# Kernel tuning notes

Measured on AMD Instinct MI355X. Metric: run time of the kernel, lower is better.

The kernel has to match this reference:

```python
import jax, jax.numpy as jnp
import numpy as np
import math

B, N, F_IN, F_OUT = 16, 2048, 256, 64


def setup_inputs() -> dict:
    key = jax.random.key(0)
    k1, k2, k3, k4 = jax.random.split(key, 4)
    x = jax.random.normal(k1, (B, N, F_IN), dtype=jnp.float32)
    adj = jax.random.randint(k2, (B, N, N), 0, 2, dtype=jnp.int32)
    stdv = 1.0 / math.sqrt(F_OUT)
    weight = jax.random.uniform(k3, (F_IN, F_OUT), dtype=jnp.float32, minval=-stdv, maxval=stdv)
    # weight2 stdv = 1/sqrt(1) = 1.0
    weight2 = jax.random.uniform(k4, (2 * F_OUT, 1), dtype=jnp.float32, minval=-1.0, maxval=1.0)
    return {"x": x, "adj": adj, "weight": weight, "weight2": weight2}


def reference(x, adj, weight, weight2):
    # h[b,n,o] = (x @ weight)  -- shared linear projection
    h = jnp.einsum("bni,io->bno", x, weight)
    Fo = weight.shape[1]
    # Split additive-attention vector: e_ij = relu(h_i . a_src + h_j . a_dst)
    # Mathematically identical to cat([h_i, h_j]) @ weight2 of the original.
    a_src = weight2[:Fo, 0]
    a_dst = weight2[Fo:, 0]
    s_src = jnp.einsum("bno,o->bn", h, a_src)  # [B, N]
    s_dst = jnp.einsum("bno,o->bn", h, a_dst)  # [B, N]
    e = jax.nn.relu(s_src[:, :, None] + s_dst[:, None, :])  # [B, N, N]
    NEG = jnp.float32(-9e15)
    scores = jnp.where(adj > 0, e, NEG)
    attention = jax.nn.softmax(scores, axis=2)  # softmax over neighbors j
    # dropout = 0.0 / eval mode -> identity
    out = jnp.einsum("bij,bjo->bio", attention, h)  # [B, N, F_OUT]
    return out
```

## Files before the change

### kernel.cpp

```cpp
#include <hip/hip_runtime.h>
#include <hip/hip_bf16.h>

#define BB 16
#define NN 2048
#define FIN 256
#define FO 64
#define CH 256
#define HSTR 264

typedef __bf16 bf16x8 __attribute__((ext_vector_type(8)));
typedef float  f32x4  __attribute__((ext_vector_type(4)));
typedef int    i32x4  __attribute__((ext_vector_type(4)));
typedef unsigned int uint;

__global__ __launch_bounds__(256) void k1_gemm(
    const float* __restrict__ x, const float* __restrict__ weight,
    const float* __restrict__ w2,
    __bf16* __restrict__ hT, float* __restrict__ s_src, float* __restrict__ s_dst) {
    __shared__ __bf16 WtL[FO * 264];
    __shared__ float vsL[FIN], vdL[FIN];
    int t = threadIdx.x;
    {
        const float4* wr = (const float4*)(weight + t * FO);
        float a = 0.f, d = 0.f;
#pragma unroll
        for (int c = 0; c < 16; ++c) {
            float4 v = wr[c];
            int o = c * 4;
            WtL[(o + 0) * 264 + t] = (__bf16)v.x;
            WtL[(o + 1) * 264 + t] = (__bf16)v.y;
            WtL[(o + 2) * 264 + t] = (__bf16)v.z;
            WtL[(o + 3) * 264 + t] = (__bf16)v.w;
            a += v.x * w2[o] + v.y * w2[o + 1] + v.z * w2[o + 2] + v.w * w2[o + 3];
            d += v.x * w2[FO + o] + v.y * w2[FO + o + 1] +
                 v.z * w2[FO + o + 2] + v.w * w2[FO + o + 3];
        }
        vsL[t] = a;
        vdL[t] = d;
    }
    __syncthreads();

    int lane = threadIdx.x & 63, w = threadIdx.x >> 6;
    int quad = lane >> 4, m = lane & 15;
    int Rbase = blockIdx.x * 64 + w * 16;
    int R = Rbase + m;
    const float* xr = x + (long)R * FIN;

    f32x4 acc[4] = {};
    float ps = 0.f, pd = 0.f;

#pragma unroll
    for (int k0 = 0; k0 < FIN; k0 += 32) {
        int kb = k0 + quad * 8;
        float4 x0 = *(const float4*)(xr + kb);
        float4 x1 = *(const float4*)(xr + kb + 4);
        float4 u0 = *(const float4*)(vsL + kb);
        float4 u1 = *(const float4*)(vsL + kb + 4);
        float4 t0 = *(const float4*)(vdL + kb);
        float4 t1 = *(const float4*)(vdL + kb + 4);
        ps += x0.x * u0.x + x0.y * u0.y + x0.z * u0.z + x0.w * u0.w +
              x1.x * u1.x + x1.y * u1.y + x1.z * u1.z + x1.w * u1.w;
        pd += x0.x * t0.x + x0.y * t0.y + x0.z * t0.z + x0.w * t0.w +
              x1.x * t1.x + x1.y * t1.y + x1.z * t1.z + x1.w * t1.w;
        bf16x8 bf = {(__bf16)x0.x, (__bf16)x0.y, (__bf16)x0.z, (__bf16)x0.w,
                     (__bf16)x1.x, (__bf16)x1.y, (__bf16)x1.z, (__bf16)x1.w};
#pragma unroll
        for (int ot = 0; ot < 4; ++ot) {
            bf16x8 af = *(const bf16x8*)(WtL + (ot * 16 + m) * 264 + kb);
            acc[ot] = __builtin_amdgcn_mfma_f32_16x16x32_bf16(af, bf, acc[ot], 0, 0, 0);
        }
    }
    ps += __shfl_xor(ps, 16);
    ps += __shfl_xor(ps, 32);
    pd += __shfl_xor(pd, 16);
    pd += __shfl_xor(pd, 32);
    if (quad == 0) {
        s_src[R] = ps;
        s_dst[R] = pd;
    }
    int b = R >> 11;
    int nb = Rbase & (NN - 1);
#pragma unroll
    for (int ot = 0; ot < 4; ++ot) {
#pragma unroll
        for (int r = 0; r < 4; ++r) {
            int o = ot * 16 + quad * 4 + r;
            hT[((long)b * FO + o) * NN + nb + m] = (__bf16)acc[ot][r];
        }
    }
}

__global__ __launch_bounds__(256, 2) void k2_attn(
    const int* __restrict__ adj, const float* __restrict__ s_src,
    const float* __restrict__ s_dst, const __bf16* __restrict__ hT,
    float* __restrict__ out) {
    __shared__ __bf16 hL[2][FO * HSTR];
    __shared__ float EL[NN];
    int b = blockIdx.x >> 5;
    int i0 = (blockIdx.x & 31) << 6;
    int lane = threadIdx.x & 63, w = threadIdx.x >> 6;
    int quad = lane >> 4, m = lane & 15;
    int rowbase = i0 + w * 16;
    int row = rowbase + m;

    const float* sd = s_dst + b * NN;
    float mx = -3.0e38f;
    for (int j = lane; j < NN; j += 64) mx = fmaxf(mx, sd[j]);
#pragma unroll
    for (int off = 32; off >= 1; off >>= 1) mx = fmaxf(mx, __shfl_xor(mx, off));
    {
        int j0 = threadIdx.x * 8;
        float4 v0 = *(const float4*)(sd + j0);
        float4 v1 = *(const float4*)(sd + j0 + 4);
        EL[j0 + 0] = __expf(v0.x - mx);
        EL[j0 + 1] = __expf(v0.y - mx);
        EL[j0 + 2] = __expf(v0.z - mx);
        EL[j0 + 3] = __expf(v0.w - mx);
        EL[j0 + 4] = __expf(v1.x - mx);
        EL[j0 + 5] = __expf(v1.y - mx);
        EL[j0 + 6] = __expf(v1.z - mx);
        EL[j0 + 7] = __expf(v1.w - mx);
    }

    float cK = __expf(-(s_src[b * NN + row] + mx));

    const i32x4* arow = (const i32x4*)(adj + ((size_t)(b * NN + row)) * NN);
    int aq = quad * 2;

    int so = threadIdx.x >> 2;
    int sc = (threadIdx.x & 3) * 64;
    const __bf16* hsrc = hT + ((long)b * FO + so) * NN + sc;
    int ldoff = so * HSTR + sc;
    int q8 = quad * 8;

    i32x4 A[16];
#pragma unroll
    for (int u = 0; u < 8; ++u) {
        A[2 * u]     = arow[u * 8 + aq];
        A[2 * u + 1] = arow[u * 8 + aq + 1];
    }
    bf16x8 st[8];
    {
        const bf16x8* sp = (const bf16x8*)hsrc;
#pragma unroll
        for (int i = 0; i < 8; ++i) st[i] = sp[i];
    }
    {
        bf16x8* dp = (bf16x8*)(hL[0] + ldoff);
#pragma unroll
        for (int i = 0; i < 8; ++i) dp[i] = st[i];
    }
    __syncthreads();

    f32x4 acc[4] = {};
    f32x4 accL = {};
    const bf16x8 ones = {(__bf16)1.f, (__bf16)1.f, (__bf16)1.f, (__bf16)1.f,
                         (__bf16)1.f, (__bf16)1.f, (__bf16)1.f, (__bf16)1.f};

    for (int c = 0; c < NN / CH; ++c) {
        const __bf16* cur = hL[c & 1];
        bf16x8 af[8];
#pragma unroll
        for (int u = 0; u < 8; ++u) {
            const float* ep = EL + (c * 8 + u) * 32 + q8;
            float4 e0 = *(const float4*)ep;
            float4 e1 = *(const float4*)(ep + 4);
            i32x4 a0 = A[2 * u], a1 = A[2 * u + 1];
            float p0 = (a0.x > 0) ? fmaxf(e0.x, cK) : 0.f;
            float p1 = (a0.y > 0) ? fmaxf(e0.y, cK) : 0.f;
            float p2 = (a0.z > 0) ? fmaxf(e0.z, cK) : 0.f;
            float p3 = (a0.w > 0) ? fmaxf(e0.w, cK) : 0.f;
            float p4 = (a1.x > 0) ? fmaxf(e1.x, cK) : 0.f;
            float p5 = (a1.y > 0) ? fmaxf(e1.y, cK) : 0.f;
            float p6 = (a1.z > 0) ? fmaxf(e1.z, cK) : 0.f;
            float p7 = (a1.w > 0) ? fmaxf(e1.w, cK) : 0.f;
            af[u] = bf16x8{(__bf16)p0, (__bf16)p1, (__bf16)p2, (__bf16)p3,
                           (__bf16)p4, (__bf16)p5, (__bf16)p6, (__bf16)p7};
        }
        if (c < NN / CH - 1) {
            const i32x4* an = arow + (c + 1) * 64;
#pragma unroll
            for (int u = 0; u < 8; ++u) {
                A[2 * u]     = an[u * 8 + aq];
                A[2 * u + 1] = an[u * 8 + aq + 1];
            }
            const bf16x8* sp = (const bf16x8*)(hsrc + (c + 1) * CH);
#pragma unroll
            for (int i = 0; i < 8; ++i) st[i] = sp[i];
        }
#pragma unroll
        for (int u = 0; u < 8; ++u) {
            accL = __builtin_amdgcn_mfma_f32_16x16x32_bf16(af[u], ones, accL, 0, 0, 0);
            const __bf16* hb = cur + u * 32 + q8;
#pragma unroll
            for (int ot = 0; ot < 4; ++ot) {
                bf16x8 bf = *(const bf16x8*)(hb + (ot * 16 + m) * HSTR);
                acc[ot] = __builtin_amdgcn_mfma_f32_16x16x32_bf16(af[u], bf, acc[ot], 0, 0, 0);
            }
        }
        if (c < NN / CH - 1) {
            bf16x8* dp = (bf16x8*)(hL[(c + 1) & 1] + ldoff);
#pragma unroll
            for (int i = 0; i < 8; ++i) dp[i] = st[i];
        }
        __syncthreads();
    }

    float* outp = out + ((long)b * NN + rowbase) * FO;
#pragma unroll
    for (int r = 0; r < 4; ++r) {
        int orow = quad * 4 + r;
        float inv = 1.0f / accL[r];
#pragma unroll
        for (int ot = 0; ot < 4; ++ot) {
            outp[(long)orow * FO + ot * 16 + m] = acc[ot][r] * inv;
        }
    }
}

extern "C" void kernel_launch(void* const* d_in, const int* in_sizes, int n_in,
                              void* d_out, int out_size, void* d_ws, size_t ws_size,
                              hipStream_t stream) {
    const float* x      = (const float*)d_in[0];
    const int*   adj    = (const int*)d_in[1];
    const float* weight = (const float*)d_in[2];
    const float* w2     = (const float*)d_in[3];
    float* out = (float*)d_out;

    char* ws = (char*)d_ws;
    __bf16* hT   = (__bf16*)ws;
    float* s_src = (float*)(ws + 4194304);
    float* s_dst = (float*)(ws + 4194304 + 131072);

    k1_gemm<<<512, 256, 0, stream>>>(x, weight, w2, hT, s_src, s_dst);
    k2_attn<<<512, 256, 0, stream>>>(adj, s_src, s_dst, hT, out);
}
```

Baseline: 393.9 us.

## Use single-wave blocks reading h directly from global, drop LDS staging

The attention kernel now runs one 64-thread wave per block covering 16 rows, with 2048 blocks remapped so consecutive blocks spread across batches. The shared-memory double buffer for h and its per-chunk barriers are removed, and B fragments are loaded straight from global/L2. Adjacency rows are prefetched with a two-register ping-pong in 128-column chunks. This removes the barrier and LDS-copy overhead and raises block count, at the cost of more redundant global reads of h per row tile and recomputing the s_dst max/exp table in every block.

```diff
diff --git a/kernel.cpp b/kernel.cpp
--- a/kernel.cpp
+++ b/kernel.cpp
@@ -5,13 +5,10 @@
 #define NN 2048
 #define FIN 256
 #define FO 64
-#define CH 256
-#define HSTR 264
 
 typedef __bf16 bf16x8 __attribute__((ext_vector_type(8)));
 typedef float  f32x4  __attribute__((ext_vector_type(4)));
 typedef int    i32x4  __attribute__((ext_vector_type(4)));
-typedef unsigned int uint;
 
 __global__ __launch_bounds__(256) void k1_gemm(
     const float* __restrict__ x, const float* __restrict__ weight,
@@ -90,121 +87,114 @@
     }
 }
 
-__global__ __launch_bounds__(256, 2) void k2_attn(
+__global__ __launch_bounds__(64, 2) void k2_attn(
     const int* __restrict__ adj, const float* __restrict__ s_src,
     const float* __restrict__ s_dst, const __bf16* __restrict__ hT,
     float* __restrict__ out) {
-    __shared__ __bf16 hL[2][FO * HSTR];
     __shared__ float EL[NN];
-    int b = blockIdx.x >> 5;
-    int i0 = (blockIdx.x & 31) << 6;
-    int lane = threadIdx.x & 63, w = threadIdx.x >> 6;
+    int bid = blockIdx.x;
+    bid = ((bid & 7) << 8) | (bid >> 3);
+    int b = bid >> 7;
+    int rowbase = (bid & 127) << 4;
+    int lane = threadIdx.x & 63;
     int quad = lane >> 4, m = lane & 15;
-    int rowbase = i0 + w * 16;
     int row = rowbase + m;
+
+    const i32x4* arow = (const i32x4*)(adj + ((size_t)(b * NN + row)) * NN) + quad * 2;
+    i32x4 A0[8], A1[8];
+#pragma unroll
+    for (int u = 0; u < 4; ++u) {
+        A0[2 * u]     = arow[u * 8];
+        A0[2 * u + 1] = arow[u * 8 + 1];
+    }
 
     const float* sd = s_dst + b * NN;
     float mx = -3.0e38f;
     for (int j = lane; j < NN; j += 64) mx = fmaxf(mx, sd[j]);
 #pragma unroll
     for (int off = 32; off >= 1; off >>= 1) mx = fmaxf(mx, __shfl_xor(mx, off));
-    {
-        int j0 = threadIdx.x * 8;
-        float4 v0 = *(const float4*)(sd + j0);
-        float4 v1 = *(const float4*)(sd + j0 + 4);
-        EL[j0 + 0] = __expf(v0.x - mx);
-        EL[j0 + 1] = __expf(v0.y - mx);
-        EL[j0 + 2] = __expf(v0.z - mx);
-        EL[j0 + 3] = __expf(v0.w - mx);
-        EL[j0 + 4] = __expf(v1.x - mx);
-        EL[j0 + 5] = __expf(v1.y - mx);
-        EL[j0 + 6] = __expf(v1.z - mx);
-        EL[j0 + 7] = __expf(v1.w - mx);
-    }
+
+#pragma unroll
+    for (int t = 0; t < 8; ++t) {
+        int j0 = t * 256 + lane * 4;
+        float4 v = *(const float4*)(sd + j0);
+        float4 e;
+        e.x = __expf(v.x - mx);
+        e.y = __expf(v.y - mx);
+        e.z = __expf(v.z - mx);
+        e.w = __expf(v.w - mx);
+        *(float4*)(EL + j0) = e;
+    }
+    __syncthreads();
 
     float cK = __expf(-(s_src[b * NN + row] + mx));
 
-    const i32x4* arow = (const i32x4*)(adj + ((size_t)(b * NN + row)) * NN);
-    int aq = quad * 2;
-
-    int so = threadIdx.x >> 2;
-    int sc = (threadIdx.x & 3) * 64;
-    const __bf16* hsrc = hT + ((long)b * FO + so) * NN + sc;
-    int ldoff = so * HSTR + sc;
-    int q8 = quad * 8;
-
-    i32x4 A[16];
-#pragma unroll
-    for (int u = 0; u < 8; ++u) {
-        A[2 * u]     = arow[u * 8 + aq];
-        A[2 * u + 1] = arow[u * 8 + aq + 1];
-    }
-    bf16x8 st[8];
-    {
-        const bf16x8* sp = (const bf16x8*)hsrc;
-#pragma unroll
-        for (int i = 0; i < 8; ++i) st[i] = sp[i];
-    }
-    {
-        bf16x8* dp = (bf16x8*)(hL[0] + ldoff);
-#pragma unroll
-        for (int i = 0; i < 8; ++i) dp[i] = st[i];
-    }
-    __syncthreads();
+    const float* elp = EL + quad * 8;
+    const __bf16* hq = hT + ((long)b * FO + m) * NN + quad * 8;
+    const __bf16* hb0 = hq;
+    const __bf16* hb1 = hq + 16 * NN;
+    const __bf16* hb2 = hq + 32 * NN;
+    const __bf16* hb3 = hq + 48 * NN;
 
     f32x4 acc[4] = {};
     f32x4 accL = {};
     const bf16x8 ones = {(__bf16)1.f, (__bf16)1.f, (__bf16)1.f, (__bf16)1.f,
                          (__bf16)1.f, (__bf16)1.f, (__bf16)1.f, (__bf16)1.f};
 
-    for (int c = 0; c < NN / CH; ++c) {
-        const __bf16* cur = hL[c & 1];
-        bf16x8 af[8];
-#pragma unroll
-        for (int u = 0; u < 8; ++u) {
-            const float* ep = EL + (c * 8 + u) * 32 + q8;
-            float4 e0 = *(const float4*)ep;
-            float4 e1 = *(const float4*)(ep + 4);
-            i32x4 a0 = A[2 * u], a1 = A[2 * u + 1];
-            float p0 = (a0.x > 0) ? fmaxf(e0.x, cK) : 0.f;
-            float p1 = (a0.y > 0) ? fmaxf(e0.y, cK) : 0.f;
-            float p2 = (a0.z > 0) ? fmaxf(e0.z, cK) : 0.f;
-            float p3 = (a0.w > 0) ? fmaxf(e0.w, cK) : 0.f;
-            float p4 = (a1.x > 0) ? fmaxf(e1.x, cK) : 0.f;
-            float p5 = (a1.y > 0) ? fmaxf(e1.y, cK) : 0.f;
-            float p6 = (a1.z > 0) ? fmaxf(e1.z, cK) : 0.f;
-            float p7 = (a1.w > 0) ? fmaxf(e1.w, cK) : 0.f;
-            af[u] = bf16x8{(__bf16)p0, (__bf16)p1, (__bf16)p2, (__bf16)p3,
-                           (__bf16)p4, (__bf16)p5, (__bf16)p6, (__bf16)p7};
-        }
-        if (c < NN / CH - 1) {
-            const i32x4* an = arow + (c + 1) * 64;
-#pragma unroll
-            for (int u = 0; u < 8; ++u) {
-                A[2 * u]     = an[u * 8 + aq];
-                A[2 * u + 1] = an[u * 8 + aq + 1];
+#define COMPUTE(cc, AA)                                                          \
+    {                                                                            \
+        _Pragma("unroll") for (int u = 0; u < 4; ++u) {                          \
+            const float* ep = elp + (cc) * 128 + u * 32;                         \
+            float4 e0 = *(const float4*)ep;                                      \
+            float4 e1 = *(const float4*)(ep + 4);                                \
+            i32x4 a0 = AA[2 * u], a1 = AA[2 * u + 1];                            \
+            float p0 = (a0.x > 0) ? fmaxf(e0.x, cK) : 0.f;                       \
+            float p1 = (a0.y > 0) ? fmaxf(e0.y, cK) : 0.f;                       \
+            float p2 = (a0.z > 0) ? fmaxf(e0.z, cK) : 0.f;                       \
+            float p3 = (a0.w > 0) ? fmaxf(e0.w, cK) : 0.f;                       \
+            float p4 = (a1.x > 0) ? fmaxf(e1.x, cK) : 0.f;                       \
+            float p5 = (a1.y > 0) ? fmaxf(e1.y, cK) : 0.f;                       \
+            float p6 = (a1.z > 0) ? fmaxf(e1.z, cK) : 0.f;                       \
+            float p7 = (a1.w > 0) ? fmaxf(e1.w, cK) : 0.f;                       \
+            bf16x8 af = {(__bf16)p0, (__bf16)p1, (__bf16)p2, (__bf16)p3,         \
+                         (__bf16)p4, (__bf16)p5, (__bf16)p6, (__bf16)p7};        \
+            accL = __builtin_amdgcn_mfma_f32_16x16x32_bf16(af, ones, accL,       \
+                                                           0, 0, 0);             \
+            int jo = (cc) * 128 + u * 32;                                        \
+            bf16x8 bf0 = *(const bf16x8*)(hb0 + jo);                             \
+            acc[0] = __builtin_amdgcn_mfma_f32_16x16x32_bf16(af, bf0, acc[0],    \
+                                                             0, 0, 0);           \
+            bf16x8 bf1 = *(const bf16x8*)(hb1 + jo);                             \
+            acc[1] = __builtin_amdgcn_mfma_f32_16x16x32_bf16(af, bf1, acc[1],    \
+                                                             0, 0, 0);           \
+            bf16x8 bf2 = *(const bf16x8*)(hb2 + jo);                             \
+            acc[2] = __builtin_amdgcn_mfma_f32_16x16x32_bf16(af, bf2, acc[2],    \
+                                                             0, 0, 0);           \
+            bf16x8 bf3 = *(const bf16x8*)(hb3 + jo);                             \
+            acc[3] = __builtin_amdgcn_mfma_f32_16x16x32_bf16(af, bf3, acc[3],    \
+                                                             0, 0, 0);           \
+        }                                                                        \
+    }
+
+    for (int c = 0; c < NN / 128; c += 2) {
+        const i32x4* an = arow + (c + 1) * 32;
+#pragma unroll
+        for (int u = 0; u < 4; ++u) {
+            A1[2 * u]     = an[u * 8];
+            A1[2 * u + 1] = an[u * 8 + 1];
+        }
+        COMPUTE(c, A0);
+        if (c < NN / 128 - 2) {
+            const i32x4* an2 = arow + (c + 2) * 32;
+#pragma unroll
+            for (int u = 0; u < 4; ++u) {
+                A0[2 * u]     = an2[u * 8];
+                A0[2 * u + 1] = an2[u * 8 + 1];
             }
-            const bf16x8* sp = (const bf16x8*)(hsrc + (c + 1) * CH);
-#pragma unroll
-            for (int i = 0; i < 8; ++i) st[i] = sp[i];
-        }
-#pragma unroll
-        for (int u = 0; u < 8; ++u) {
-            accL = __builtin_amdgcn_mfma_f32_16x16x32_bf16(af[u], ones, accL, 0, 0, 0);
-            const __bf16* hb = cur + u * 32 + q8;
-#pragma unroll
-            for (int ot = 0; ot < 4; ++ot) {
-                bf16x8 bf = *(const bf16x8*)(hb + (ot * 16 + m) * HSTR);
-                acc[ot] = __builtin_amdgcn_mfma_f32_16x16x32_bf16(af[u], bf, acc[ot], 0, 0, 0);
-            }
-        }
-        if (c < NN / CH - 1) {
-            bf16x8* dp = (bf16x8*)(hL[(c + 1) & 1] + ldoff);
-#pragma unroll
-            for (int i = 0; i < 8; ++i) dp[i] = st[i];
-        }
-        __syncthreads();
-    }
+        }
+        COMPUTE(c + 1, A1);
+    }
+#undef COMPUTE
 
     float* outp = out + ((long)b * NN + rowbase) * FO;
 #pragma unroll
@@ -233,5 +223,5 @@
     float* s_dst = (float*)(ws + 4194304 + 131072);
 
     k1_gemm<<<512, 256, 0, stream>>>(x, weight, w2, hT, s_src, s_dst);
-    k2_attn<<<512, 256, 0, stream>>>(adj, s_src, s_dst, hT, out);
+    k2_attn<<<2048, 64, 0, stream>>>(adj, s_src, s_dst, hT, out);
 }
```

New measurement: 416.2 us. 1.06x slower.
